# Kernel optimization log

Measured on AMD Instinct MI355X. Metric: run time of the kernel, lower is better.

Reference implementation:

```python
import jax, jax.numpy as jnp
import numpy as np

DELTA_V = 0.5
DELTA_D = 1.5
ALPHA = 1.0
BETA = 1.0
GAMMA = 0.001
K = 64  # max number of instance ids per batch element


def _safe_sqrt(sq):
    # sqrt with zero-safe gradient: exact where sq > 0, returns 0 otherwise
    pos = sq > 0
    return jnp.sqrt(jnp.where(pos, sq, 1.0)) * pos.astype(sq.dtype)


def setup_inputs() -> dict:
    key = jax.random.key(0)
    k1, k2 = jax.random.split(key)
    B, N, D = 16, 65536, 32
    embeddings = jax.random.normal(k1, (B, N, D), dtype=jnp.float32)
    instance_ids = jax.random.randint(k2, (B, N), 0, K, dtype=jnp.int32)
    mask = jnp.ones((B, N), dtype=bool)
    return {"embeddings": embeddings, "instance_ids": instance_ids, "mask": mask}


def reference(embeddings, instance_ids, mask):
    B, N, D = embeddings.shape
    f32 = embeddings.dtype
    valid = mask & (instance_ids >= 0)
    # flat segment id per point; invalid points go to dump segment B*K
    batch_off = jnp.arange(B, dtype=jnp.int32)[:, None] * K
    seg = jnp.where(valid, batch_off + instance_ids, B * K).reshape(-1)
    w = valid.reshape(-1).astype(f32)
    flat = embeddings.reshape(-1, D)

    # per-instance sums / counts -> means  (segment reduce, memory-bound)
    sums = jax.ops.segment_sum(flat * w[:, None], seg, num_segments=B * K + 1)[: B * K]
    counts = jax.ops.segment_sum(w, seg, num_segments=B * K + 1)[: B * K]
    means_flat = sums / jnp.maximum(counts, 1.0)[:, None]  # (B*K, D)
    present = (counts > 0).reshape(B, K)                   # (B, K)
    num_inst = present.sum(-1).astype(f32)                 # (B,)
    valid_b = (num_inst >= 2).astype(f32)                  # batches counted as samples

    # ---- variance (pull) loss ----
    seg_clip = jnp.minimum(seg, B * K - 1)
    diff = flat - means_flat[seg_clip]                     # (B*N, D)
    dist = _safe_sqrt((diff * diff).sum(-1))
    pen = jnp.maximum(dist - DELTA_V, 0.0) ** 2 * w
    inst_pen = jax.ops.segment_sum(pen, seg, num_segments=B * K + 1)[: B * K]
    inst_pen = (inst_pen / jnp.maximum(counts, 1.0)).reshape(B, K)
    var_b = (inst_pen * present).sum(-1) / jnp.maximum(num_inst, 1.0)

    # ---- distance (push) loss: pairwise over instance means ----
    means = means_flat.reshape(B, K, D)
    dsq = ((means[:, :, None, :] - means[:, None, :, :]) ** 2).sum(-1)  # (B, K, K)
    iu = jnp.arange(K)
    pair_m = present[:, :, None] & present[:, None, :] & (iu[:, None] < iu[None, :])
    pair_mf = pair_m.astype(f32)
    pdist = _safe_sqrt(jnp.where(pair_m, dsq, 1.0)) * pair_mf
    pen2 = jnp.maximum(2.0 * DELTA_D - pdist, 0.0) ** 2 * pair_mf
    num_pairs = num_inst * (num_inst - 1.0) / 2.0
    dist_b = pen2.sum((1, 2)) / jnp.maximum(num_pairs, 1.0)

    # ---- regularization loss ----
    mnorm = _safe_sqrt((means * means).sum(-1)) * present.astype(f32)  # (B, K)
    reg_b = mnorm.sum(-1) / jnp.maximum(num_inst, 1.0)

    denom = jnp.maximum(valid_b.sum(), 1.0)
    var_loss = (var_b * valid_b).sum() / denom
    dist_loss = (dist_b * valid_b).sum() / denom
    reg_loss = (reg_b * valid_b).sum() / denom
    total = ALPHA * var_loss + BETA * dist_loss + GAMMA * reg_loss
    return jnp.stack([total, var_loss, dist_loss, reg_loss])
```

## Files before the change

kernel.cpp:

```cpp
#include <hip/hip_runtime.h>
#include <cstdint>

#define BB 16
#define NN 65536
#define DD 32
#define KK 64
#define DELTA_V 0.5f
#define DELTA_D 1.5f

typedef short bf16x8 __attribute__((ext_vector_type(8)));
typedef float f32x16 __attribute__((ext_vector_type(16)));

__device__ __forceinline__ short f2bf(float x) {
    union { float f; unsigned u; } v; v.f = x;
    const unsigned r = v.u + 0x7FFFu + ((v.u >> 16) & 1u);
    return (short)(r >> 16);
}

#define K1_BPB 64
#define K1_PTS (NN / K1_BPB)
#define K1_WPTS (K1_PTS / 4)

__global__ __launch_bounds__(256) void k_accum(
    const float* __restrict__ emb, const int* __restrict__ ids,
    const int* __restrict__ mask, float* __restrict__ sums,
    float* __restrict__ counts)
{
    __shared__ float lws[4][KK][DD];
    __shared__ int   lcnt[4][KK];
    __shared__ int   lid[4][64];
    const int tid  = threadIdx.x;
    const int w    = tid >> 6, lane = tid & 63;
    const int half = lane >> 5, d32 = lane & 31;
    const int b    = blockIdx.x >> 6;
    const int blk  = blockIdx.x & 63;
    const size_t pw = (size_t)b * NN + (size_t)blk * K1_PTS + (size_t)w * K1_WPTS;

    f32x16 acc0 = {}, acc1 = {};
    int c0 = 0, c1 = 0;
    const int m0 = d32, m1 = d32 + 32;

    for (int c = 0; c < K1_WPTS; c += 64) {
        const int idraw = ids[pw + c + lane];
        const int mk    = mask[pw + c + lane];
        lid[w][lane] = (mk != 0 && (unsigned)idraw < KK) ? idraw : -1;

#pragma unroll
        for (int q = 0; q < 4; ++q) {
            const size_t P0 = pw + c + q * 16 + half * 8;
            const float* eb = emb + P0 * DD + d32;
            float xe[8];
#pragma unroll
            for (int e = 0; e < 8; ++e) xe[e] = eb[(size_t)e * DD];

            const int* lp = &lid[w][q * 16 + half * 8];
            bf16x8 bf, a0, a1;
#pragma unroll
            for (int e = 0; e < 8; ++e) {
                const int idv = lp[e];
                bf[e] = f2bf(xe[e]);
                const bool h0 = (idv == m0), h1 = (idv == m1);
                a0[e] = h0 ? (short)0x3F80 : (short)0;
                a1[e] = h1 ? (short)0x3F80 : (short)0;
                c0 += h0 ? 1 : 0;
                c1 += h1 ? 1 : 0;
            }
            acc0 = __builtin_amdgcn_mfma_f32_32x32x16_bf16(a0, bf, acc0, 0, 0, 0);
            acc1 = __builtin_amdgcn_mfma_f32_32x32x16_bf16(a1, bf, acc1, 0, 0, 0);
        }
    }

#pragma unroll
    for (int r = 0; r < 16; ++r) {
        const int mrow = (r & 3) + 8 * (r >> 2) + 4 * half;
        lws[w][mrow][d32]      = acc0[r];
        lws[w][32 + mrow][d32] = acc1[r];
    }
    c0 += __shfl_down(c0, 32);
    c1 += __shfl_down(c1, 32);
    if (lane < 32) { lcnt[w][lane] = c0; lcnt[w][lane + 32] = c1; }
    __syncthreads();

    float* gs = sums + (size_t)b * KK * DD;
    for (int i = tid; i < KK * DD; i += 256) {
        const float s = ((const float*)lws[0])[i] + ((const float*)lws[1])[i]
                      + ((const float*)lws[2])[i] + ((const float*)lws[3])[i];
        atomicAdd(&gs[i], s);
    }
    if (tid < KK)
        atomicAdd(&counts[b * KK + tid],
                  (float)(lcnt[0][tid] + lcnt[1][tid] + lcnt[2][tid] + lcnt[3][tid]));
}

#define K2_BPB 64
#define K2_PTS (NN / K2_BPB)

__global__ __launch_bounds__(128) void k_pull(
    const float* __restrict__ emb, const int* __restrict__ ids,
    const int* __restrict__ mask, const float* __restrict__ sums,
    const float* __restrict__ counts, float* __restrict__ ipen)
{
    __shared__ float mu[DD][KK];
    __shared__ float lpp[128][KK + 1];
    const int tid = threadIdx.x;
    const int b   = blockIdx.x >> 6;
    const int blk = blockIdx.x & 63;

    const float* gs = sums + (size_t)b * KK * DD;
    const float* gc = counts + b * KK;
    for (int i = tid; i < KK * DD; i += 128) {
        const int k = i & 63, dd = i >> 6;
        mu[dd][k] = gs[k * DD + dd] / fmaxf(gc[k], 1.f);
    }
    for (int i = tid; i < 128 * (KK + 1); i += 128) ((float*)lpp)[i] = 0.f;
    __syncthreads();

    const size_t p0 = (size_t)b * NN + (size_t)blk * K2_PTS;
    float* myrow = lpp[tid];
    for (int p = tid; p < K2_PTS; p += 128) {
        const int id = ids[p0 + p];
        const bool v = (mask[p0 + p] != 0) && ((unsigned)id < KK);
        const int sid = v ? id : 0;
        const float4* e = (const float4*)(emb + (p0 + p) * DD);
        float dsq = 0.f;
#pragma unroll
        for (int q = 0; q < 8; ++q) {
            const float4 t = e[q];
            float a;
            a = t.x - mu[4 * q + 0][sid]; dsq = fmaf(a, a, dsq);
            a = t.y - mu[4 * q + 1][sid]; dsq = fmaf(a, a, dsq);
            a = t.z - mu[4 * q + 2][sid]; dsq = fmaf(a, a, dsq);
            a = t.w - mu[4 * q + 3][sid]; dsq = fmaf(a, a, dsq);
        }
        const float dist = (dsq > 0.f) ? sqrtf(dsq) : 0.f;
        float pen = fmaxf(dist - DELTA_V, 0.f);
        pen = pen * pen;
        if (v) myrow[sid] += pen;
    }
    __syncthreads();
    if (tid < KK) {
        float s = 0.f;
        for (int r = 0; r < 128; ++r) s += lpp[r][tid];
        atomicAdd(&ipen[b * KK + tid], s);
    }
}

__global__ __launch_bounds__(256) void k_push_reg(
    const float* __restrict__ sums, const float* __restrict__ counts,
    float* __restrict__ regb, float* __restrict__ distb)
{
    const int b = blockIdx.x;
    const int tid = threadIdx.x;
    __shared__ float lm[KK][DD + 1];
    __shared__ float lcnt[KK];
    __shared__ float red[4];

    if (tid < KK) lcnt[tid] = counts[b * KK + tid];
    __syncthreads();

    const float* gs = sums + (size_t)b * KK * DD;
    for (int i = tid; i < KK * DD; i += 256) {
        const int k = i >> 5, d = i & 31;
        lm[k][d] = gs[i] / fmaxf(lcnt[k], 1.f);
    }
    __syncthreads();

    float ninst = 0.f;
    if (tid < KK) {
        const float c = lcnt[tid];
        const float pres = (c > 0.f) ? 1.f : 0.f;
        float sq = 0.f;
#pragma unroll
        for (int d = 0; d < DD; ++d) { const float m = lm[tid][d]; sq = fmaf(m, m, sq); }
        float nm = ((sq > 0.f) ? sqrtf(sq) : 0.f) * pres;
        float pn = pres;
        for (int off = 32; off; off >>= 1) {
            pn += __shfl_down(pn, off);
            nm += __shfl_down(nm, off);
        }
        if (tid == 0) {
            ninst = pn;
            regb[b] = nm / fmaxf(pn, 1.f);
        }
    }

    float acc = 0.f;
    for (int idx = tid; idx < KK * KK; idx += 256) {
        const int i = idx >> 6, j = idx & 63;
        if (i < j && lcnt[i] > 0.f && lcnt[j] > 0.f) {
            float dsq = 0.f;
#pragma unroll
            for (int d = 0; d < DD; ++d) {
                const float df = lm[i][d] - lm[j][d];
                dsq = fmaf(df, df, dsq);
            }
            const float pd = (dsq > 0.f) ? sqrtf(dsq) : 0.f;
            const float pen = fmaxf(2.f * DELTA_D - pd, 0.f);
            acc = fmaf(pen, pen, acc);
        }
    }
    for (int off = 32; off; off >>= 1) acc += __shfl_down(acc, off);
    if ((tid & 63) == 0) red[tid >> 6] = acc;
    __syncthreads();
    if (tid == 0) {
        const float tot = red[0] + red[1] + red[2] + red[3];
        const float np = ninst * (ninst - 1.f) * 0.5f;
        distb[b] = tot / fmaxf(np, 1.f);
    }
}

__global__ __launch_bounds__(64) void k_final(
    const float* __restrict__ counts, const float* __restrict__ inst_pen,
    const float* __restrict__ regb, const float* __restrict__ distb,
    float* __restrict__ out)
{
    const int tid = threadIdx.x;
    __shared__ float s_var[BB], s_valid[BB];
    if (tid < BB) {
        const int b = tid;
        float vn = 0.f, ni = 0.f;
        for (int k = 0; k < KK; ++k) {
            const float c = counts[b * KK + k];
            if (c > 0.f) { ni += 1.f; vn += inst_pen[b * KK + k] / c; }
        }
        s_var[tid]   = vn / fmaxf(ni, 1.f);
        s_valid[tid] = (ni >= 2.f) ? 1.f : 0.f;
    }
    __syncthreads();
    if (tid == 0) {
        float denom = 0.f, v = 0.f, d = 0.f, r = 0.f;
        for (int b = 0; b < BB; ++b) {
            const float vb = s_valid[b];
            denom += vb;
            v += s_var[b] * vb;
            d += distb[b] * vb;
            r += regb[b] * vb;
        }
        denom = fmaxf(denom, 1.f);
        v /= denom; d /= denom; r /= denom;
        out[0] = v + d + 0.001f * r;
        out[1] = v;
        out[2] = d;
        out[3] = r;
    }
}

extern "C" void kernel_launch(void* const* d_in, const int* in_sizes, int n_in,
                              void* d_out, int out_size, void* d_ws, size_t ws_size,
                              hipStream_t stream)
{
    const float* emb  = (const float*)d_in[0];
    const int*   ids  = (const int*)d_in[1];
    const int*   mask = (const int*)d_in[2];

    float* ws     = (float*)d_ws;
    float* sums   = ws;
    float* counts = sums + (size_t)BB * KK * DD;
    float* ipen   = counts + BB * KK;
    float* regb   = ipen + BB * KK;
    float* distb  = regb + BB;

    hipMemsetAsync(sums, 0, (size_t)(BB * KK * DD + 2 * BB * KK) * sizeof(float),
                   stream);

    k_accum<<<BB * K1_BPB, 256, 0, stream>>>(emb, ids, mask, sums, counts);
    k_pull<<<BB * K2_BPB, 128, 0, stream>>>(emb, ids, mask, sums, counts, ipen);
    k_push_reg<<<BB, 256, 0, stream>>>(sums, counts, regb, distb);
    k_final<<<1, 64, 0, stream>>>(counts, ipen, regb, distb, (float*)d_out);
}
```

Before: 98.90 us.

## Replace atomic segment sums with per-block partials, reduce kernel, and LDS-direct loads

The accumulation kernel now runs one wavefront per block over 512 points and stages embeddings into LDS with global_load_lds. Each block writes its own partial sums and counts instead of issuing atomicAdds, and a new reduce kernel sums the partials into precomputed means with the count packed alongside. The pull kernel reads these means from a padded row and folds the division by count into one per-batch scalar accumulator, which removes the 128x65 LDS per-instance penalty table and its final reduction. The cost is about 17 MB of partial-buffer traffic, an extra kernel launch, and a vmcnt(0) wait after each LDS-staged load.

```diff
diff --git a/kernel.cpp b/kernel.cpp
--- a/kernel.cpp
+++ b/kernel.cpp
@@ -17,137 +17,162 @@
     return (short)(r >> 16);
 }
 
-#define K1_BPB 64
-#define K1_PTS (NN / K1_BPB)
-#define K1_WPTS (K1_PTS / 4)
-
-__global__ __launch_bounds__(256) void k_accum(
+__device__ __forceinline__ void gll16(const float* g, float* l) {
+    __builtin_amdgcn_global_load_lds(
+        (const __attribute__((address_space(1))) unsigned int*)g,
+        (__attribute__((address_space(3))) unsigned int*)l, 16, 0, 0);
+}
+
+#define K1_BLOCKS 2048
+#define K1_PPB 512
+
+__global__ __launch_bounds__(64) void k_accum(
     const float* __restrict__ emb, const int* __restrict__ ids,
-    const int* __restrict__ mask, float* __restrict__ sums,
-    float* __restrict__ counts)
-{
-    __shared__ float lws[4][KK][DD];
-    __shared__ int   lcnt[4][KK];
-    __shared__ int   lid[4][64];
-    const int tid  = threadIdx.x;
-    const int w    = tid >> 6, lane = tid & 63;
+    const int* __restrict__ mask, float* __restrict__ parts,
+    float* __restrict__ pcnt)
+{
+    __shared__ float ebuf[32][32];
+    const int lane = threadIdx.x;
     const int half = lane >> 5, d32 = lane & 31;
-    const int b    = blockIdx.x >> 6;
-    const int blk  = blockIdx.x & 63;
-    const size_t pw = (size_t)b * NN + (size_t)blk * K1_PTS + (size_t)w * K1_WPTS;
+    const int blk  = blockIdx.x;
+    const int b    = blk >> 7;
+    const size_t p0 = (size_t)b * NN + (size_t)(blk & 127) * K1_PPB;
 
     f32x16 acc0 = {}, acc1 = {};
     int c0 = 0, c1 = 0;
     const int m0 = d32, m1 = d32 + 32;
 
-    for (int c = 0; c < K1_WPTS; c += 64) {
-        const int idraw = ids[pw + c + lane];
-        const int mk    = mask[pw + c + lane];
-        lid[w][lane] = (mk != 0 && (unsigned)idraw < KK) ? idraw : -1;
-
-#pragma unroll
-        for (int q = 0; q < 4; ++q) {
-            const size_t P0 = pw + c + q * 16 + half * 8;
-            const float* eb = emb + P0 * DD + d32;
-            float xe[8];
-#pragma unroll
-            for (int e = 0; e < 8; ++e) xe[e] = eb[(size_t)e * DD];
-
-            const int* lp = &lid[w][q * 16 + half * 8];
-            bf16x8 bf, a0, a1;
-#pragma unroll
-            for (int e = 0; e < 8; ++e) {
-                const int idv = lp[e];
-                bf[e] = f2bf(xe[e]);
-                const bool h0 = (idv == m0), h1 = (idv == m1);
-                a0[e] = h0 ? (short)0x3F80 : (short)0;
-                a1[e] = h1 ? (short)0x3F80 : (short)0;
-                c0 += h0 ? 1 : 0;
-                c1 += h1 ? 1 : 0;
+    for (int s = 0; s < K1_PPB / 64; ++s) {
+        const size_t ps = p0 + s * 64;
+        const int idr = ids[ps + lane];
+        const int mkr = mask[ps + lane];
+        const int vid = (mkr != 0 && (unsigned)idr < KK) ? idr : -1;
+#pragma unroll
+        for (int h = 0; h < 2; ++h) {
+            const float* gsrc = emb + (ps + h * 32) * DD;
+#pragma unroll
+            for (int i = 0; i < 4; ++i)
+                gll16(gsrc + i * 256 + lane * 4, &ebuf[0][0] + i * 256);
+            asm volatile("s_waitcnt vmcnt(0)" ::: "memory");
+            __builtin_amdgcn_sched_barrier(0);
+#pragma unroll
+            for (int q = 0; q < 2; ++q) {
+                bf16x8 bfB, a0, a1;
+#pragma unroll
+                for (int e = 0; e < 8; ++e) {
+                    const int pt = q * 16 + 8 * half + e;
+                    bfB[e] = f2bf(ebuf[pt][d32]);
+                    const int s_lo = __builtin_amdgcn_readlane(vid, h * 32 + q * 16 + e);
+                    const int s_hi = __builtin_amdgcn_readlane(vid, h * 32 + q * 16 + 8 + e);
+                    const int sel  = half ? s_hi : s_lo;
+                    const bool h0 = (sel == m0), h1 = (sel == m1);
+                    a0[e] = h0 ? (short)0x3F80 : (short)0;
+                    a1[e] = h1 ? (short)0x3F80 : (short)0;
+                    c0 += h0 ? 1 : 0;
+                    c1 += h1 ? 1 : 0;
+                }
+                acc0 = __builtin_amdgcn_mfma_f32_32x32x16_bf16(a0, bfB, acc0, 0, 0, 0);
+                acc1 = __builtin_amdgcn_mfma_f32_32x32x16_bf16(a1, bfB, acc1, 0, 0, 0);
             }
-            acc0 = __builtin_amdgcn_mfma_f32_32x32x16_bf16(a0, bf, acc0, 0, 0, 0);
-            acc1 = __builtin_amdgcn_mfma_f32_32x32x16_bf16(a1, bf, acc1, 0, 0, 0);
-        }
-    }
-
+        }
+    }
+
+    float* pb = parts + (size_t)blk * (KK * DD);
 #pragma unroll
     for (int r = 0; r < 16; ++r) {
         const int mrow = (r & 3) + 8 * (r >> 2) + 4 * half;
-        lws[w][mrow][d32]      = acc0[r];
-        lws[w][32 + mrow][d32] = acc1[r];
+        pb[mrow * DD + d32]        = acc0[r];
+        pb[(32 + mrow) * DD + d32] = acc1[r];
     }
     c0 += __shfl_down(c0, 32);
     c1 += __shfl_down(c1, 32);
-    if (lane < 32) { lcnt[w][lane] = c0; lcnt[w][lane + 32] = c1; }
-    __syncthreads();
-
-    float* gs = sums + (size_t)b * KK * DD;
-    for (int i = tid; i < KK * DD; i += 256) {
-        const float s = ((const float*)lws[0])[i] + ((const float*)lws[1])[i]
-                      + ((const float*)lws[2])[i] + ((const float*)lws[3])[i];
-        atomicAdd(&gs[i], s);
-    }
-    if (tid < KK)
-        atomicAdd(&counts[b * KK + tid],
-                  (float)(lcnt[0][tid] + lcnt[1][tid] + lcnt[2][tid] + lcnt[3][tid]));
+    if (lane < 32) {
+        pcnt[(size_t)blk * KK + lane]      = (float)c0;
+        pcnt[(size_t)blk * KK + 32 + lane] = (float)c1;
+    }
+}
+
+__global__ __launch_bounds__(128) void k_reduce(
+    const float* __restrict__ parts, const float* __restrict__ pcnt,
+    float* __restrict__ mu)
+{
+    const int b = blockIdx.x >> 4;
+    const int c = blockIdx.x & 15;
+    const int tid = threadIdx.x;
+    __shared__ float t4[128][4];
+    __shared__ float scnt[4];
+
+    const float* pc = pcnt + (size_t)b * 128 * KK + c * 4;
+#pragma unroll
+    for (int u = 0; u < 4; ++u) t4[tid][u] = pc[(size_t)tid * KK + u];
+    __syncthreads();
+    if (tid < 4) {
+        float s = 0.f;
+        for (int j = 0; j < 128; ++j) s += t4[j][tid];
+        scnt[tid] = s;
+    }
+    __syncthreads();
+
+    const int e = c * 128 + tid;
+    const float* pp = parts + (size_t)b * 128 * (KK * DD) + e;
+    float s = 0.f;
+    for (int j = 0; j < 128; ++j) s += pp[(size_t)j * (KK * DD)];
+    const int k = e >> 5, d = e & 31;
+    const float cnt = scnt[tid >> 5];
+    mu[(size_t)b * KK * 33 + k * 33 + d] = s / fmaxf(cnt, 1.f);
+    if (tid < 4) mu[(size_t)b * KK * 33 + (c * 4 + tid) * 33 + 32] = scnt[tid];
 }
 
 #define K2_BPB 64
 #define K2_PTS (NN / K2_BPB)
 
-__global__ __launch_bounds__(128) void k_pull(
+__global__ __launch_bounds__(256) void k_pull(
     const float* __restrict__ emb, const int* __restrict__ ids,
-    const int* __restrict__ mask, const float* __restrict__ sums,
-    const float* __restrict__ counts, float* __restrict__ ipen)
-{
-    __shared__ float mu[DD][KK];
-    __shared__ float lpp[128][KK + 1];
+    const int* __restrict__ mask, const float* __restrict__ mu,
+    float* __restrict__ varacc)
+{
+    __shared__ float smu[KK * 33];
+    __shared__ float red[4];
     const int tid = threadIdx.x;
     const int b   = blockIdx.x >> 6;
     const int blk = blockIdx.x & 63;
 
-    const float* gs = sums + (size_t)b * KK * DD;
-    const float* gc = counts + b * KK;
-    for (int i = tid; i < KK * DD; i += 128) {
-        const int k = i & 63, dd = i >> 6;
-        mu[dd][k] = gs[k * DD + dd] / fmaxf(gc[k], 1.f);
-    }
-    for (int i = tid; i < 128 * (KK + 1); i += 128) ((float*)lpp)[i] = 0.f;
+    const float* mub = mu + (size_t)b * KK * 33;
+    for (int i = tid; i < KK * 33; i += 256) smu[i] = mub[i];
     __syncthreads();
 
     const size_t p0 = (size_t)b * NN + (size_t)blk * K2_PTS;
-    float* myrow = lpp[tid];
-    for (int p = tid; p < K2_PTS; p += 128) {
+    float accv = 0.f;
+    for (int p = tid; p < K2_PTS; p += 256) {
         const int id = ids[p0 + p];
         const bool v = (mask[p0 + p] != 0) && ((unsigned)id < KK);
         const int sid = v ? id : 0;
+        const float* mr = smu + sid * 33;
         const float4* e = (const float4*)(emb + (p0 + p) * DD);
         float dsq = 0.f;
 #pragma unroll
         for (int q = 0; q < 8; ++q) {
             const float4 t = e[q];
             float a;
-            a = t.x - mu[4 * q + 0][sid]; dsq = fmaf(a, a, dsq);
-            a = t.y - mu[4 * q + 1][sid]; dsq = fmaf(a, a, dsq);
-            a = t.z - mu[4 * q + 2][sid]; dsq = fmaf(a, a, dsq);
-            a = t.w - mu[4 * q + 3][sid]; dsq = fmaf(a, a, dsq);
+            a = t.x - mr[4 * q + 0]; dsq = fmaf(a, a, dsq);
+            a = t.y - mr[4 * q + 1]; dsq = fmaf(a, a, dsq);
+            a = t.z - mr[4 * q + 2]; dsq = fmaf(a, a, dsq);
+            a = t.w - mr[4 * q + 3]; dsq = fmaf(a, a, dsq);
         }
         const float dist = (dsq > 0.f) ? sqrtf(dsq) : 0.f;
         float pen = fmaxf(dist - DELTA_V, 0.f);
         pen = pen * pen;
-        if (v) myrow[sid] += pen;
-    }
-    __syncthreads();
-    if (tid < KK) {
-        float s = 0.f;
-        for (int r = 0; r < 128; ++r) s += lpp[r][tid];
-        atomicAdd(&ipen[b * KK + tid], s);
-    }
+        if (v) accv += pen / fmaxf(mr[32], 1.f);
+    }
+    for (int off = 32; off; off >>= 1) accv += __shfl_down(accv, off);
+    if ((tid & 63) == 0) red[tid >> 6] = accv;
+    __syncthreads();
+    if (tid == 0) atomicAdd(&varacc[b], red[0] + red[1] + red[2] + red[3]);
 }
 
 __global__ __launch_bounds__(256) void k_push_reg(
-    const float* __restrict__ sums, const float* __restrict__ counts,
-    float* __restrict__ regb, float* __restrict__ distb)
+    const float* __restrict__ mu, float* __restrict__ regb,
+    float* __restrict__ distb)
 {
     const int b = blockIdx.x;
     const int tid = threadIdx.x;
@@ -155,14 +180,12 @@
     __shared__ float lcnt[KK];
     __shared__ float red[4];
 
-    if (tid < KK) lcnt[tid] = counts[b * KK + tid];
-    __syncthreads();
-
-    const float* gs = sums + (size_t)b * KK * DD;
+    const float* mub = mu + (size_t)b * KK * 33;
     for (int i = tid; i < KK * DD; i += 256) {
         const int k = i >> 5, d = i & 31;
-        lm[k][d] = gs[i] / fmaxf(lcnt[k], 1.f);
-    }
+        lm[k][d] = mub[k * 33 + d];
+    }
+    if (tid < KK) lcnt[tid] = mub[tid * 33 + 32];
     __syncthreads();
 
     float ninst = 0.f;
@@ -210,7 +233,7 @@
 }
 
 __global__ __launch_bounds__(64) void k_final(
-    const float* __restrict__ counts, const float* __restrict__ inst_pen,
+    const float* __restrict__ mu, const float* __restrict__ varacc,
     const float* __restrict__ regb, const float* __restrict__ distb,
     float* __restrict__ out)
 {
@@ -218,12 +241,10 @@
     __shared__ float s_var[BB], s_valid[BB];
     if (tid < BB) {
         const int b = tid;
-        float vn = 0.f, ni = 0.f;
-        for (int k = 0; k < KK; ++k) {
-            const float c = counts[b * KK + k];
-            if (c > 0.f) { ni += 1.f; vn += inst_pen[b * KK + k] / c; }
-        }
-        s_var[tid]   = vn / fmaxf(ni, 1.f);
+        float ni = 0.f;
+        for (int k = 0; k < KK; ++k)
+            ni += (mu[(size_t)b * KK * 33 + k * 33 + 32] > 0.f) ? 1.f : 0.f;
+        s_var[tid]   = varacc[b] / fmaxf(ni, 1.f);
         s_valid[tid] = (ni >= 2.f) ? 1.f : 0.f;
     }
     __syncthreads();
@@ -254,17 +275,18 @@
     const int*   mask = (const int*)d_in[2];
 
     float* ws     = (float*)d_ws;
-    float* sums   = ws;
-    float* counts = sums + (size_t)BB * KK * DD;
-    float* ipen   = counts + BB * KK;
-    float* regb   = ipen + BB * KK;
+    float* parts  = ws;
+    float* pcnt   = parts + (size_t)K1_BLOCKS * KK * DD;
+    float* mu     = pcnt + (size_t)K1_BLOCKS * KK;
+    float* varacc = mu + (size_t)BB * KK * 33;
+    float* regb   = varacc + BB;
     float* distb  = regb + BB;
 
-    hipMemsetAsync(sums, 0, (size_t)(BB * KK * DD + 2 * BB * KK) * sizeof(float),
-                   stream);
-
-    k_accum<<<BB * K1_BPB, 256, 0, stream>>>(emb, ids, mask, sums, counts);
-    k_pull<<<BB * K2_BPB, 128, 0, stream>>>(emb, ids, mask, sums, counts, ipen);
-    k_push_reg<<<BB, 256, 0, stream>>>(sums, counts, regb, distb);
-    k_final<<<1, 64, 0, stream>>>(counts, ipen, regb, distb, (float*)d_out);
-}
+    hipMemsetAsync(varacc, 0, BB * sizeof(float), stream);
+
+    k_accum<<<K1_BLOCKS, 64, 0, stream>>>(emb, ids, mask, parts, pcnt);
+    k_reduce<<<BB * 16, 128, 0, stream>>>(parts, pcnt, mu);
+    k_pull<<<BB * K2_BPB, 256, 0, stream>>>(emb, ids, mask, mu, varacc);
+    k_push_reg<<<BB, 256, 0, stream>>>(mu, regb, distb);
+    k_final<<<1, 64, 0, stream>>>(mu, varacc, regb, distb, (float*)d_out);
+}
```

New measurement: 94.35 us. 1.05x faster.
